# Kernel optimization log

Measured on AMD Instinct MI355X. Metric: run time of the kernel, lower is better.

Reference implementation:

```python
import jax, jax.numpy as jnp
import numpy as np

B_, H_, W_, C_ = 4, 128, 128, 256
HEADS = 8
SPLIT = (8, 32)
POS_DIM = ((C_ // 2) // 4) // 4  # DynamicPosBias(dim//4).pos_dim with dim=C//2 -> 8


def _rel_tables(Hsp, Wsp):
    # rpe_biases: all relative (dy, dx) offsets, shape [(2Hsp-1)*(2Wsp-1), 2]
    gy, gx = np.meshgrid(np.arange(1 - Hsp, Hsp), np.arange(1 - Wsp, Wsp), indexing='ij')
    biases = np.stack([gy.ravel(), gx.ravel()], axis=1).astype(np.float32)
    # relative_position_index: [N, N] lookup into the bias table
    ch, cw = np.meshgrid(np.arange(Hsp), np.arange(Wsp), indexing='ij')
    cf = np.stack([ch.ravel(), cw.ravel()])  # [2, N]
    rel = (cf[:, :, None] - cf[:, None, :]).transpose(1, 2, 0)
    rel[..., 0] += Hsp - 1
    rel[..., 1] += Wsp - 1
    rel[..., 0] *= 2 * Wsp - 1
    idx = rel.sum(-1)
    return jnp.asarray(biases), jnp.asarray(idx)


def _ln(x, g, b):
    m = x.mean(-1, keepdims=True)
    v = ((x - m) ** 2).mean(-1, keepdims=True)
    return (x - m) / jnp.sqrt(v + 1e-5) * g + b


def _dyn_pos(biases, pw, pb, g1, b1, w1, c1, g2, b2, w2, c2, g3, b3, w3, c3):
    # DynamicPosBias, residual=False: pos3(pos2(pos1(pos_proj(b))))
    p = biases @ pw + pb
    p = jax.nn.relu(_ln(p, g1, b1)) @ w1 + c1
    p = jax.nn.relu(_ln(p, g2, b2)) @ w2 + c2
    p = jax.nn.relu(_ln(p, g3, b3)) @ w3 + c3
    return p  # [num_rel, heads]


def _win_attn(q, k, v, Hsp, Wsp, H, W, heads, pos_table, rel_idx):
    B, L, Cb = q.shape
    N = Hsp * Wsp
    hd = Cb // heads
    scale = hd ** (-0.5)

    def part(t):  # (B, L, Cb) -> (B*nW, heads, N, hd)
        t = t.reshape(B, H // Hsp, Hsp, W // Wsp, Wsp, Cb)
        t = t.transpose(0, 1, 3, 2, 4, 5).reshape(-1, N, heads, hd)
        return t.transpose(0, 2, 1, 3)

    qw, kw, vw = part(q) * scale, part(k), part(v)
    attn = jnp.einsum('whnd,whmd->whnm', qw, kw)
    rpb = pos_table[rel_idx.reshape(-1)].reshape(N, N, heads).transpose(2, 0, 1)
    attn = jax.nn.softmax(attn + rpb[None], axis=-1)
    ow = jnp.einsum('whnm,whmd->whnd', attn, vw)
    ow = ow.transpose(0, 2, 1, 3).reshape(-1, N, Cb)
    # windows2img
    img = ow.reshape(B, H // Hsp, W // Wsp, Hsp, Wsp, Cb)
    img = img.transpose(0, 1, 3, 2, 4, 5).reshape(B, H * W, Cb)
    return img


def setup_inputs() -> dict:
    key = jax.random.key(0)
    ks = jax.random.split(key, 16)
    nrm = lambda k, shp: jax.random.normal(k, shp, jnp.float32) * 0.02
    P, hb = POS_DIM, HEADS // 2
    d = {}
    d['x'] = jax.random.normal(ks[0], (B_, H_ * W_, C_), jnp.float32)
    d['w_qkv'] = nrm(ks[1], (C_, 3 * C_))
    d['w_proj'] = nrm(ks[2], (C_, C_))
    d['b_proj'] = jnp.zeros((C_,), jnp.float32)
    d['w_dw'] = nrm(ks[3], (C_, 1, 3, 3))
    d['b_dw'] = jnp.zeros((C_,), jnp.float32)
    d['pp_w'] = nrm(ks[4], (2, 2, P))
    d['pp_b'] = jnp.zeros((2, P), jnp.float32)
    d['ln1_g'] = jnp.ones((2, P), jnp.float32)
    d['ln1_b'] = jnp.zeros((2, P), jnp.float32)
    d['l1_w'] = nrm(ks[5], (2, P, P))
    d['l1_b'] = jnp.zeros((2, P), jnp.float32)
    d['ln2_g'] = jnp.ones((2, P), jnp.float32)
    d['ln2_b'] = jnp.zeros((2, P), jnp.float32)
    d['l2_w'] = nrm(ks[6], (2, P, P))
    d['l2_b'] = jnp.zeros((2, P), jnp.float32)
    d['ln3_g'] = jnp.ones((2, P), jnp.float32)
    d['ln3_b'] = jnp.zeros((2, P), jnp.float32)
    d['l3_w'] = nrm(ks[7], (2, P, hb))
    d['l3_b'] = jnp.zeros((2, hb), jnp.float32)
    d['H'] = H_
    d['W'] = W_
    return d


def reference(x, w_qkv, w_proj, b_proj, w_dw, b_dw, pp_w, pp_b, ln1_g, ln1_b, l1_w, l1_b, ln2_g, ln2_b, l2_w, l2_b, ln3_g, ln3_b, l3_w, l3_b, H, W):
    B, L, C = x.shape
    Cb, hb = C // 2, HEADS // 2
    qkv = (x @ w_qkv).reshape(B, L, 3, C).transpose(2, 0, 1, 3)
    q, k, v = qkv[0], qkv[1], qkv[2]
    v_img = v.transpose(0, 2, 1).reshape(B, C, H, W)
    outs = []
    for br in range(2):  # two cross-shaped window branches (idx=0/1)
        Hsp, Wsp = SPLIT if br == 0 else (SPLIT[1], SPLIT[0])
        sl = slice(br * Cb, (br + 1) * Cb)
        biases, rel_idx = _rel_tables(Hsp, Wsp)
        pos = _dyn_pos(biases, pp_w[br], pp_b[br], ln1_g[br], ln1_b[br], l1_w[br], l1_b[br],
                       ln2_g[br], ln2_b[br], l2_w[br], l2_b[br], ln3_g[br], ln3_b[br], l3_w[br], l3_b[br])
        outs.append(_win_attn(q[..., sl], k[..., sl], v[..., sl], Hsp, Wsp, H, W, hb, pos, rel_idx))
    att = jnp.concatenate(outs, axis=-1)  # (B, L, C)
    # LePE: depthwise 3x3 conv on V (get_v, groups=dim)
    lepe = jax.lax.conv_general_dilated(v_img, w_dw, (1, 1), ((1, 1), (1, 1)),
                                        feature_group_count=C,
                                        dimension_numbers=('NCHW', 'OIHW', 'NCHW'))
    lepe = (lepe + b_dw[None, :, None, None]).transpose(0, 2, 3, 1).reshape(B, L, C)
    return (att + lepe) @ w_proj + b_proj
```

## Files before the change

kernel.cpp:

```cpp
#include <hip/hip_runtime.h>
#include <hip/hip_bf16.h>
#include <math.h>

#define B_ 4
#define HH 128
#define WW 128
#define CC 256
#define LL (HH * WW)
#define NROWS (B_ * LL)
#define NREL 945
#define SCALE 0.17677669529663687f
#define LOG2E 1.4426950408889634f
#define SCALE2 (0.17677669529663687f * 1.4426950408889634f)

typedef __attribute__((ext_vector_type(8))) _Float16 half8;
typedef __attribute__((ext_vector_type(2))) __fp16 fp16x2;
typedef __attribute__((ext_vector_type(4))) float f32x4;

__device__ __forceinline__ unsigned short f2h(float f) {
    union { _Float16 h; unsigned short u; } v;
    v.h = (_Float16)f;
    return v.u;
}
__device__ __forceinline__ float h2f(unsigned short u) {
    union { unsigned short u; _Float16 h; } v;
    v.u = u;
    return (float)v.h;
}
__device__ __forceinline__ float exp2_raw(float x) {
    float r;
    asm("v_exp_f32 %0, %1" : "=v"(r) : "v"(x));
    return r;
}
__device__ __forceinline__ void gl_lds16(const unsigned short* g, unsigned short* l) {
    __builtin_amdgcn_global_load_lds((const __attribute__((address_space(1))) void*)g,
                                     (__attribute__((address_space(3))) void*)l, 16, 0, 0);
}

__device__ inline void ln_relu8(float* v, const float* g, const float* b) {
    float m = 0.f;
#pragma unroll
    for (int j = 0; j < 8; j++) m += v[j];
    m *= 0.125f;
    float var = 0.f;
#pragma unroll
    for (int j = 0; j < 8; j++) { float d = v[j] - m; var += d * d; }
    var *= 0.125f;
    float inv = 1.0f / sqrtf(var + 1e-5f);
#pragma unroll
    for (int j = 0; j < 8; j++) {
        float xn = (v[j] - m) * inv * g[j] + b[j];
        v[j] = xn > 0.f ? xn : 0.f;
    }
}

__device__ inline void mat8x8(const float* in, float* out, const float* w, const float* bias) {
#pragma unroll
    for (int j = 0; j < 8; j++) {
        float s = bias[j];
#pragma unroll
        for (int i = 0; i < 8; i++) s = fmaf(in[i], w[i * 8 + j], s);
        out[j] = s;
    }
}

__global__ void pos_kernel(const float* __restrict__ pp_w, const float* __restrict__ pp_b,
                           const float* __restrict__ ln1_g, const float* __restrict__ ln1_b,
                           const float* __restrict__ l1_w, const float* __restrict__ l1_b,
                           const float* __restrict__ ln2_g, const float* __restrict__ ln2_b,
                           const float* __restrict__ l2_w, const float* __restrict__ l2_b,
                           const float* __restrict__ ln3_g, const float* __restrict__ ln3_b,
                           const float* __restrict__ l3_w, const float* __restrict__ l3_b,
                           float* __restrict__ pos) {
    const int br = blockIdx.x;
    const int Wsp = br ? 8 : 32;
    const int Hsp = br ? 32 : 8;
    const int W2 = 2 * Wsp - 1;
    const int nrel = (2 * Hsp - 1) * W2;
    for (int r = threadIdx.x; r < nrel; r += blockDim.x) {
        float dy = (float)(r / W2 - (Hsp - 1));
        float dx = (float)(r % W2 - (Wsp - 1));
        float p[8], t[8];
#pragma unroll
        for (int j = 0; j < 8; j++)
            p[j] = dy * pp_w[br * 16 + j] + dx * pp_w[br * 16 + 8 + j] + pp_b[br * 8 + j];
        ln_relu8(p, ln1_g + br * 8, ln1_b + br * 8);
        mat8x8(p, t, l1_w + br * 64, l1_b + br * 8);
        ln_relu8(t, ln2_g + br * 8, ln2_b + br * 8);
        mat8x8(t, p, l2_w + br * 64, l2_b + br * 8);
        ln_relu8(p, ln3_g + br * 8, ln3_b + br * 8);
#pragma unroll
        for (int j = 0; j < 4; j++) {
            float s = l3_b[br * 4 + j];
#pragma unroll
            for (int i = 0; i < 8; i++) s = fmaf(p[i], l3_w[br * 32 + i * 4 + j], s);
            pos[(br * NREL + r) * 4 + j] = s;
        }
    }
}

__global__ void rpb_kernel(const float* __restrict__ pos, float* __restrict__ T2) {
    const int m = threadIdx.x;
    const int n = blockIdx.x;
    const int h = blockIdx.y;
    const int br = blockIdx.z;
    const int logW = br ? 3 : 5;
    const int Wsp = 1 << logW;
    const int Hsp = 256 >> logW;
    const int W2 = 2 * Wsp - 1;
    const int i_n = n >> logW, j_n = n & (Wsp - 1);
    const int i_m = m >> logW, j_m = m & (Wsp - 1);
    const int idx = (i_n - i_m + Hsp - 1) * W2 + (j_n - j_m + Wsp - 1);
    float v = pos[(br * NREL + idx) * 4 + h] * LOG2E;
    const int qs = n >> 4;
    const int ks = m >> 4;
    const int lane = ((n >> 2) & 3) * 16 + (m & 15);
    const int i = n & 3;
    T2[((((size_t)(br * 4 + h) * 16 + qs) * 16 + ks) * 64 + lane) * 4 + i] = v;
}

__global__ void convw_kernel(const float* __restrict__ w, unsigned short* __restrict__ th,
                             int Kd, int Nd) {
    int idx = blockIdx.x * blockDim.x + threadIdx.x;
    if (idx >= Kd * Nd) return;
    int n = idx / Kd, k = idx - n * Kd;
    th[idx] = f2h(w[(size_t)k * Nd + n]);
}

__global__ __launch_bounds__(256) void convx_kernel(const float* __restrict__ x,
                                                    unsigned short* __restrict__ xh) {
    size_t i = ((size_t)blockIdx.x * 256 + threadIdx.x) * 4;
    float4 v = *(const float4*)(x + i);
    ushort4 h;
    h.x = f2h(v.x); h.y = f2h(v.y); h.z = f2h(v.z); h.w = f2h(v.w);
    *(ushort4*)(xh + i) = h;
}

__global__ __launch_bounds__(256) void gemm_f16(const unsigned short* __restrict__ A,
                                                const unsigned short* __restrict__ B,
                                                unsigned short* __restrict__ C,
                                                int ldc, int nblk) {
    const int K = 256;
    __shared__ unsigned short sA[4096];
    __shared__ unsigned short sB[4096];

    const int tid = threadIdx.x;
    const int cpx = gridDim.x >> 3;
    const int bid = blockIdx.x;
    const int swz = (bid & 7) * cpx + (bid >> 3);
    const int nb = swz % nblk;
    const int mb = swz / nblk;
    const size_t blockM = (size_t)mb * 128;
    const int blockN = nb * 128;

    const int srow = tid >> 2;
    const int schunk = (tid & 3) * 8;
    const unsigned short* pA = A + (blockM + srow) * K + schunk;
    const unsigned short* pB = B + (size_t)(blockN + srow) * K + schunk;
    const size_t rstep = (size_t)64 * K;

    const int w = tid >> 6;
    const int lane = tid & 63;
    const int quad = lane >> 4;
    const int l15 = lane & 15;
    const int wm = (w & 1) * 64;
    const int wn = (w >> 1) * 64;

    f32x4 acc[4][4];
#pragma unroll
    for (int i = 0; i < 4; i++)
#pragma unroll
        for (int j = 0; j < 4; j++) acc[i][j] = (f32x4){0.f, 0.f, 0.f, 0.f};

    for (int kb = 0; kb < K; kb += 32) {
        gl_lds16(pA + kb, sA + tid * 8);
        gl_lds16(pA + kb + rstep, sA + 2048 + tid * 8);
        gl_lds16(pB + kb, sB + tid * 8);
        gl_lds16(pB + kb + rstep, sB + 2048 + tid * 8);
        __syncthreads();

        half8 fa[4], fb[4];
#pragma unroll
        for (int i = 0; i < 4; i++) {
            fa[i] = *(const half8*)(sA + (wm + i * 16 + l15) * 32 + quad * 8);
            fb[i] = *(const half8*)(sB + (wn + i * 16 + l15) * 32 + quad * 8);
        }
#pragma unroll
        for (int i = 0; i < 4; i++)
#pragma unroll
            for (int j = 0; j < 4; j++)
                acc[i][j] = __builtin_amdgcn_mfma_f32_16x16x32_f16(fa[i], fb[j], acc[i][j], 0, 0, 0);
        __syncthreads();
    }

#pragma unroll
    for (int j = 0; j < 4; j++) {
        int col = blockN + wn + j * 16 + l15;
        float sc = (ldc == 768 && col < 256) ? SCALE2 : 1.0f;
#pragma unroll
        for (int i = 0; i < 4; i++)
#pragma unroll
            for (int r = 0; r < 4; r++) {
                size_t row = blockM + wm + i * 16 + quad * 4 + r;
                C[row * ldc + col] = f2h(acc[i][j][r] * sc);
            }
    }
}

__global__ __launch_bounds__(256) void gemm_proj(const unsigned short* __restrict__ A,
                                                 const unsigned short* __restrict__ B,
                                                 float* __restrict__ C,
                                                 const float* __restrict__ bias) {
    const int K = 256;
    __shared__ unsigned short sA[4096];
    __shared__ unsigned short sB[4096];

    const int tid = threadIdx.x;
    const int cpx = gridDim.x >> 3;
    const int bid = blockIdx.x;
    const int swz = (bid & 7) * cpx + (bid >> 3);
    const int nb = swz & 1;
    const int mb = swz >> 1;
    const size_t blockM = (size_t)mb * 128;
    const int blockN = nb * 128;

    const int srow = tid >> 2;
    const int schunk = (tid & 3) * 8;
    const unsigned short* pA = A + (blockM + srow) * K + schunk;
    const unsigned short* pB = B + (size_t)(blockN + srow) * K + schunk;
    const size_t rstep = (size_t)64 * K;

    const int w = tid >> 6;
    const int lane = tid & 63;
    const int quad = lane >> 4;
    const int l15 = lane & 15;
    const int wm = (w & 1) * 64;
    const int wn = (w >> 1) * 64;

    f32x4 acc[4][4];
#pragma unroll
    for (int i = 0; i < 4; i++)
#pragma unroll
        for (int j = 0; j < 4; j++) acc[i][j] = (f32x4){0.f, 0.f, 0.f, 0.f};

    for (int kb = 0; kb < K; kb += 32) {
        gl_lds16(pA + kb, sA + tid * 8);
        gl_lds16(pA + kb + rstep, sA + 2048 + tid * 8);
        gl_lds16(pB + kb, sB + tid * 8);
        gl_lds16(pB + kb + rstep, sB + 2048 + tid * 8);
        __syncthreads();

        half8 fa[4], fb[4];
#pragma unroll
        for (int i = 0; i < 4; i++) {
            fa[i] = *(const half8*)(sA + (wm + i * 16 + l15) * 32 + quad * 8);
            fb[i] = *(const half8*)(sB + (wn + i * 16 + l15) * 32 + quad * 8);
        }
#pragma unroll
        for (int i = 0; i < 4; i++)
#pragma unroll
            for (int j = 0; j < 4; j++)
                acc[i][j] = __builtin_amdgcn_mfma_f32_16x16x32_f16(fa[i], fb[j], acc[i][j], 0, 0, 0);
        __syncthreads();
    }

#pragma unroll
    for (int j = 0; j < 4; j++) {
        int col = blockN + wn + j * 16 + l15;
        float bv = bias[col];
#pragma unroll
        for (int i = 0; i < 4; i++)
#pragma unroll
            for (int r = 0; r < 4; r++) {
                size_t row = blockM + wm + i * 16 + quad * 4 + r;
                C[row * 256 + col] = acc[i][j][r] + bv;
            }
    }
}

__global__ __launch_bounds__(256) void attn_mfma(const unsigned short* __restrict__ qkvb,
                                                 const float* __restrict__ T2,
                                                 unsigned short* __restrict__ attb) {
    __shared__ unsigned short Ks[256][32];
    __shared__ unsigned short Vt[32][264];
    __shared__ unsigned int   Pc[4][16][20];

    const int tid = threadIdx.x;
    const int wi = blockIdx.x;
    const int h = blockIdx.y;
    const int br = blockIdx.z;
    const int logW = br ? 3 : 5;
    const int Wsp = 1 << logW;
    const int Hsp = 256 >> logW;
    const int logNWx = br ? 4 : 2;
    const int b = wi >> 6;
    const int win = wi & 63;
    const int wy = win >> logNWx;
    const int wx = win & ((1 << logNWx) - 1);
    const int ccol = br * 128 + h * 32;

#pragma unroll
    for (int it = 0; it < 8; ++it) {
        int n = it * 32 + (tid >> 3);
        int d4 = (tid & 7) * 4;
        int iy = n >> logW, ix = n & (Wsp - 1);
        size_t row = ((size_t)b * LL + (wy * Hsp + iy) * WW + wx * Wsp + ix) * 768;
        ushort4 kv = *(const ushort4*)(qkvb + row + 256 + ccol + d4);
        ushort4 vv = *(const ushort4*)(qkvb + row + 512 + ccol + d4);
        *(ushort4*)&Ks[n][d4] = kv;
        int pos = (n & ~31) + 2 * (n & 15) + ((n >> 4) & 1);
        Vt[d4 + 0][pos] = vv.x;
        Vt[d4 + 1][pos] = vv.y;
        Vt[d4 + 2][pos] = vv.z;
        Vt[d4 + 3][pos] = vv.w;
    }
    __syncthreads();

    const int w = tid >> 6;
    const int lane = tid & 63;
    const int quad = lane >> 4;
    const int l15 = lane & 15;
    const f32x4 zero = {0.f, 0.f, 0.f, 0.f};

#pragma unroll 1
    for (int qt = 0; qt < 4; ++qt) {
        const int qbase = qt * 64 + w * 16;
        const int qrow = qbase + l15;
        const int iyq = qrow >> logW, ixq = qrow & (Wsp - 1);
        const size_t qpix = (size_t)b * LL + (wy * Hsp + iyq) * WW + wx * Wsp + ixq;
        half8 qfrag = *(const half8*)(qkvb + qpix * 768 + ccol + quad * 8);

        const float* Tf = T2 + (((size_t)(br * 4 + h) * 16 + (qt * 4 + w)) * 16) * 256 + lane * 4;

        f32x4 o0 = zero, o1 = zero;
        float rsum[4] = {0.f, 0.f, 0.f, 0.f};

#pragma unroll 2
        for (int kc = 0; kc < 8; ++kc) {
            const int kb0 = kc * 32;
            f32x4 b0 = *(const f32x4*)(Tf + (size_t)(kc * 2) * 256);
            f32x4 b1 = *(const f32x4*)(Tf + (size_t)(kc * 2 + 1) * 256);
            half8 kf0 = *(const half8*)&Ks[kb0 + l15][quad * 8];
            half8 kf1 = *(const half8*)&Ks[kb0 + 16 + l15][quad * 8];
            f32x4 s0 = __builtin_amdgcn_mfma_f32_16x16x32_f16(qfrag, kf0, b0, 0, 0, 0);
            f32x4 s1 = __builtin_amdgcn_mfma_f32_16x16x32_f16(qfrag, kf1, b1, 0, 0, 0);
#pragma unroll
            for (int i = 0; i < 4; ++i) {
                float e0 = exp2_raw(s0[i]);
                float e1 = exp2_raw(s1[i]);
                rsum[i] += e0 + e1;
                union { fp16x2 h; unsigned u; } cv;
                cv.h = __builtin_amdgcn_cvt_pkrtz(e0, e1);
                Pc[w][quad * 4 + i][l15] = cv.u;
            }
            half8 pf = *(const half8*)&Pc[w][l15][quad * 4];
            half8 vf0 = *(const half8*)&Vt[l15][kb0 + quad * 8];
            half8 vf1 = *(const half8*)&Vt[16 + l15][kb0 + quad * 8];
            o0 = __builtin_amdgcn_mfma_f32_16x16x32_f16(pf, vf0, o0, 0, 0, 0);
            o1 = __builtin_amdgcn_mfma_f32_16x16x32_f16(pf, vf1, o1, 0, 0, 0);
        }

#pragma unroll
        for (int i = 0; i < 4; ++i) {
            float s = rsum[i];
            s += __shfl_xor(s, 1, 64);
            s += __shfl_xor(s, 2, 64);
            s += __shfl_xor(s, 4, 64);
            s += __shfl_xor(s, 8, 64);
            rsum[i] = 1.0f / s;
        }

#pragma unroll
        for (int i = 0; i < 4; ++i) {
            int r = qbase + quad * 4 + i;
            int iyr = r >> logW, ixr = r & (Wsp - 1);
            size_t pix = (size_t)b * LL + (wy * Hsp + iyr) * WW + wx * Wsp + ixr;
            unsigned short* op = attb + pix * 256 + ccol;
            op[l15] = f2h(o0[i] * rsum[i]);
            op[16 + l15] = f2h(o1[i] * rsum[i]);
        }
    }
}

__global__ __launch_bounds__(256) void lepe_kernel(const unsigned short* __restrict__ qkvb,
                                                   const float* __restrict__ w_dw,
                                                   const float* __restrict__ b_dw,
                                                   unsigned short* __restrict__ attb) {
    const int lane = threadIdx.x & 63;
    const int wv = threadIdx.x >> 6;
    const int c4 = lane * 4;
    const int gid = blockIdx.x * 4 + wv;
    const int ys = gid & 7;
    const int x  = (gid >> 3) & 127;
    const int b  = gid >> 10;
    const int y0 = ys * 16;

    float wreg[36];
    const float* wp = w_dw + c4 * 9;
#pragma unroll
    for (int q = 0; q < 9; q++) {
        float4 t = *(const float4*)(wp + q * 4);
        wreg[q * 4 + 0] = t.x; wreg[q * 4 + 1] = t.y;
        wreg[q * 4 + 2] = t.z; wreg[q * 4 + 3] = t.w;
    }
    const float4 bv = *(const float4*)(b_dw + c4);
    const float4 z4 = {0.f, 0.f, 0.f, 0.f};
    const bool xm_ok = (x > 0), xp_ok = (x < 127);

    const unsigned short* vp = qkvb + (((size_t)b << 14) + x) * 768 + 512 + c4;

    float4 r0[3], r1[3], r2[3];

#define LDV(yy, dx, dst) { \
        ushort4 u = *(const ushort4*)(vp + (ptrdiff_t)(yy) * 98304 + (dx) * 768); \
        dst.x = h2f(u.x); dst.y = h2f(u.y); dst.z = h2f(u.z); dst.w = h2f(u.w); }
#define LDROW(yy, d) { \
        if ((yy) < 0 || (yy) > 127) { d[0] = z4; d[1] = z4; d[2] = z4; } \
        else { \
            if (xm_ok) LDV(yy, -1, d[0]) else d[0] = z4; \
            LDV(yy, 0, d[1]); \
            if (xp_ok) LDV(yy, 1, d[2]) else d[2] = z4; } }
#define TAP(rv, j) \
        acc.x = fmaf(rv.x, wreg[0 * 9 + (j)], acc.x); \
        acc.y = fmaf(rv.y, wreg[1 * 9 + (j)], acc.y); \
        acc.z = fmaf(rv.z, wreg[2 * 9 + (j)], acc.z); \
        acc.w = fmaf(rv.w, wreg[3 * 9 + (j)], acc.w);

    LDROW(y0 - 1, r0)
    LDROW(y0, r1)

#pragma unroll
    for (int t = 0; t < 16; ++t) {
        const int y = y0 + t;
        LDROW(y + 1, r2)

        const size_t opx = ((((size_t)b << 14) + y * 128 + x) << 8) + c4;
        ushort4 av = *(const ushort4*)(attb + opx);
        float4 acc;
        acc.x = h2f(av.x) + bv.x; acc.y = h2f(av.y) + bv.y;
        acc.z = h2f(av.z) + bv.z; acc.w = h2f(av.w) + bv.w;

        TAP(r0[0], 0) TAP(r0[1], 1) TAP(r0[2], 2)
        TAP(r1[0], 3) TAP(r1[1], 4) TAP(r1[2], 5)
        TAP(r2[0], 6) TAP(r2[1], 7) TAP(r2[2], 8)

        ushort4 o;
        o.x = f2h(acc.x); o.y = f2h(acc.y); o.z = f2h(acc.z); o.w = f2h(acc.w);
        *(ushort4*)(attb + opx) = o;

        r0[0] = r1[0]; r0[1] = r1[1]; r0[2] = r1[2];
        r1[0] = r2[0]; r1[1] = r2[1]; r1[2] = r2[2];
    }
#undef LDV
#undef LDROW
#undef TAP
}

extern "C" void kernel_launch(void* const* d_in, const int* in_sizes, int n_in,
                              void* d_out, int out_size, void* d_ws, size_t ws_size,
                              hipStream_t stream) {
    const float* x     = (const float*)d_in[0];
    const float* w_qkv = (const float*)d_in[1];
    const float* w_proj= (const float*)d_in[2];
    const float* b_proj= (const float*)d_in[3];
    const float* w_dw  = (const float*)d_in[4];
    const float* b_dw  = (const float*)d_in[5];
    const float* pp_w  = (const float*)d_in[6];
    const float* pp_b  = (const float*)d_in[7];
    const float* ln1_g = (const float*)d_in[8];
    const float* ln1_b = (const float*)d_in[9];
    const float* l1_w  = (const float*)d_in[10];
    const float* l1_b  = (const float*)d_in[11];
    const float* ln2_g = (const float*)d_in[12];
    const float* ln2_b = (const float*)d_in[13];
    const float* l2_w  = (const float*)d_in[14];
    const float* l2_b  = (const float*)d_in[15];
    const float* ln3_g = (const float*)d_in[16];
    const float* ln3_b = (const float*)d_in[17];
    const float* l3_w  = (const float*)d_in[18];
    const float* l3_b  = (const float*)d_in[19];

    float* pos = (float*)d_ws;
    float* T2  = pos + 7680;
    unsigned short* qkvb = (unsigned short*)(T2 + 524288);
    unsigned short* attb = qkvb + (size_t)NROWS * 768;
    unsigned short* xh   = attb + (size_t)NROWS * 256;
    unsigned short* wqh  = xh + (size_t)NROWS * 256;
    unsigned short* wph  = wqh + 768 * 256;

    pos_kernel<<<2, 128, 0, stream>>>(pp_w, pp_b, ln1_g, ln1_b, l1_w, l1_b,
                                      ln2_g, ln2_b, l2_w, l2_b, ln3_g, ln3_b,
                                      l3_w, l3_b, pos);
    rpb_kernel<<<dim3(256, 4, 2), 256, 0, stream>>>(pos, T2);
    convw_kernel<<<768, 256, 0, stream>>>(w_qkv, wqh, 256, 768);
    convw_kernel<<<256, 256, 0, stream>>>(w_proj, wph, 256, 256);
    convx_kernel<<<NROWS / 4, 256, 0, stream>>>(x, xh);
    gemm_f16<<<(NROWS / 128) * 6, 256, 0, stream>>>(xh, wqh, qkvb, 768, 6);
    attn_mfma<<<dim3(256, 4, 2), 256, 0, stream>>>(qkvb, T2, attb);
    lepe_kernel<<<1024, 256, 0, stream>>>(qkvb, w_dw, b_dw, attb);
    gemm_proj<<<(NROWS / 128) * 2, 256, 0, stream>>>(attb, wph, (float*)d_out, b_proj);
}
```

Measured before the change: 327.2 us.

## Compute transposed attention scores so P stays in registers, skipping LDS round trip

Swaps the MFMA operand order so S^T = K·Q^T is computed, which puts each query's scores in a layout that can be packed straight into the B operand of the PV MFMA. This removes the per-iteration shared-memory write and read of the probability tile (Pc) and the LDS traffic that came with it. The bias table and the V column permutation are re-laid out to match the new fragment ordering. Row sums now need only two cross-lane shuffles, and the output is written as vectorized ushort4 stores. The risk is that the remapped bias table or V permutation does not match the fragment layout exactly.

```diff
diff --git a/kernel.cpp b/kernel.cpp
--- a/kernel.cpp
+++ b/kernel.cpp
@@ -112,11 +112,15 @@
     const int i_m = m >> logW, j_m = m & (Wsp - 1);
     const int idx = (i_n - i_m + Hsp - 1) * W2 + (j_n - j_m + Wsp - 1);
     float v = pos[(br * NREL + idx) * 4 + h] * LOG2E;
-    const int qs = n >> 4;
-    const int ks = m >> 4;
-    const int lane = ((n >> 2) & 3) * 16 + (m & 15);
-    const int i = n & 3;
-    T2[((((size_t)(br * 4 + h) * 16 + qs) * 16 + ks) * 64 + lane) * 4 + i] = v;
+    const int qchunk = n >> 4;
+    const int l15q = n & 15;
+    const int kc = m >> 5;
+    const int lk = m & 31;
+    const int s = (lk >> 4) & 1;
+    const int quad = (lk & 15) >> 2;
+    const int i = lk & 3;
+    const int lane = quad * 16 + l15q;
+    T2[(((size_t)(br * 4 + h) * 16 + qchunk) * 4096) + ((kc * 2 + s) * 256) + lane * 4 + i] = v;
 }
 
 __global__ void convw_kernel(const float* __restrict__ w, unsigned short* __restrict__ th,
@@ -283,7 +287,6 @@
                                                  unsigned short* __restrict__ attb) {
     __shared__ unsigned short Ks[256][32];
     __shared__ unsigned short Vt[32][264];
-    __shared__ unsigned int   Pc[4][16][20];
 
     const int tid = threadIdx.x;
     const int wi = blockIdx.x;
@@ -308,7 +311,7 @@
         ushort4 kv = *(const ushort4*)(qkvb + row + 256 + ccol + d4);
         ushort4 vv = *(const ushort4*)(qkvb + row + 512 + ccol + d4);
         *(ushort4*)&Ks[n][d4] = kv;
-        int pos = (n & ~31) + 2 * (n & 15) + ((n >> 4) & 1);
+        int pos = (n & ~31) + (((n & 12) << 1) | ((n & 16) >> 2) | (n & 3));
         Vt[d4 + 0][pos] = vv.x;
         Vt[d4 + 1][pos] = vv.y;
         Vt[d4 + 2][pos] = vv.z;
@@ -330,55 +333,49 @@
         const size_t qpix = (size_t)b * LL + (wy * Hsp + iyq) * WW + wx * Wsp + ixq;
         half8 qfrag = *(const half8*)(qkvb + qpix * 768 + ccol + quad * 8);
 
-        const float* Tf = T2 + (((size_t)(br * 4 + h) * 16 + (qt * 4 + w)) * 16) * 256 + lane * 4;
+        const float* Tf = T2 + ((size_t)(br * 4 + h) * 16 + (qt * 4 + w)) * 4096 + lane * 4;
 
         f32x4 o0 = zero, o1 = zero;
-        float rsum[4] = {0.f, 0.f, 0.f, 0.f};
+        float rsum = 0.f;
 
 #pragma unroll 2
         for (int kc = 0; kc < 8; ++kc) {
             const int kb0 = kc * 32;
-            f32x4 b0 = *(const f32x4*)(Tf + (size_t)(kc * 2) * 256);
-            f32x4 b1 = *(const f32x4*)(Tf + (size_t)(kc * 2 + 1) * 256);
+            f32x4 b0 = *(const f32x4*)(Tf + kc * 512);
+            f32x4 b1 = *(const f32x4*)(Tf + kc * 512 + 256);
             half8 kf0 = *(const half8*)&Ks[kb0 + l15][quad * 8];
             half8 kf1 = *(const half8*)&Ks[kb0 + 16 + l15][quad * 8];
-            f32x4 s0 = __builtin_amdgcn_mfma_f32_16x16x32_f16(qfrag, kf0, b0, 0, 0, 0);
-            f32x4 s1 = __builtin_amdgcn_mfma_f32_16x16x32_f16(qfrag, kf1, b1, 0, 0, 0);
-#pragma unroll
-            for (int i = 0; i < 4; ++i) {
-                float e0 = exp2_raw(s0[i]);
-                float e1 = exp2_raw(s1[i]);
-                rsum[i] += e0 + e1;
-                union { fp16x2 h; unsigned u; } cv;
-                cv.h = __builtin_amdgcn_cvt_pkrtz(e0, e1);
-                Pc[w][quad * 4 + i][l15] = cv.u;
-            }
-            half8 pf = *(const half8*)&Pc[w][l15][quad * 4];
+            f32x4 s0 = __builtin_amdgcn_mfma_f32_16x16x32_f16(kf0, qfrag, b0, 0, 0, 0);
+            f32x4 s1 = __builtin_amdgcn_mfma_f32_16x16x32_f16(kf1, qfrag, b1, 0, 0, 0);
+            float e00 = exp2_raw(s0[0]), e01 = exp2_raw(s0[1]);
+            float e02 = exp2_raw(s0[2]), e03 = exp2_raw(s0[3]);
+            float e10 = exp2_raw(s1[0]), e11 = exp2_raw(s1[1]);
+            float e12 = exp2_raw(s1[2]), e13 = exp2_raw(s1[3]);
+            rsum += ((e00 + e01) + (e02 + e03)) + ((e10 + e11) + (e12 + e13));
+            union { half8 h; unsigned u[4]; } pt;
+            union { fp16x2 h; unsigned u; } cv;
+            cv.h = __builtin_amdgcn_cvt_pkrtz(e00, e01); pt.u[0] = cv.u;
+            cv.h = __builtin_amdgcn_cvt_pkrtz(e02, e03); pt.u[1] = cv.u;
+            cv.h = __builtin_amdgcn_cvt_pkrtz(e10, e11); pt.u[2] = cv.u;
+            cv.h = __builtin_amdgcn_cvt_pkrtz(e12, e13); pt.u[3] = cv.u;
             half8 vf0 = *(const half8*)&Vt[l15][kb0 + quad * 8];
             half8 vf1 = *(const half8*)&Vt[16 + l15][kb0 + quad * 8];
-            o0 = __builtin_amdgcn_mfma_f32_16x16x32_f16(pf, vf0, o0, 0, 0, 0);
-            o1 = __builtin_amdgcn_mfma_f32_16x16x32_f16(pf, vf1, o1, 0, 0, 0);
+            o0 = __builtin_amdgcn_mfma_f32_16x16x32_f16(vf0, pt.h, o0, 0, 0, 0);
+            o1 = __builtin_amdgcn_mfma_f32_16x16x32_f16(vf1, pt.h, o1, 0, 0, 0);
         }
 
-#pragma unroll
-        for (int i = 0; i < 4; ++i) {
-            float s = rsum[i];
-            s += __shfl_xor(s, 1, 64);
-            s += __shfl_xor(s, 2, 64);
-            s += __shfl_xor(s, 4, 64);
-            s += __shfl_xor(s, 8, 64);
-            rsum[i] = 1.0f / s;
-        }
-
-#pragma unroll
-        for (int i = 0; i < 4; ++i) {
-            int r = qbase + quad * 4 + i;
-            int iyr = r >> logW, ixr = r & (Wsp - 1);
-            size_t pix = (size_t)b * LL + (wy * Hsp + iyr) * WW + wx * Wsp + ixr;
-            unsigned short* op = attb + pix * 256 + ccol;
-            op[l15] = f2h(o0[i] * rsum[i]);
-            op[16 + l15] = f2h(o1[i] * rsum[i]);
-        }
+        rsum += __shfl_xor(rsum, 16, 64);
+        rsum += __shfl_xor(rsum, 32, 64);
+        const float rinv = 1.0f / rsum;
+
+        unsigned short* op = attb + qpix * 256 + ccol;
+        ushort4 w0, w1;
+        w0.x = f2h(o0[0] * rinv); w0.y = f2h(o0[1] * rinv);
+        w0.z = f2h(o0[2] * rinv); w0.w = f2h(o0[3] * rinv);
+        w1.x = f2h(o1[0] * rinv); w1.y = f2h(o1[1] * rinv);
+        w1.z = f2h(o1[2] * rinv); w1.w = f2h(o1[3] * rinv);
+        *(ushort4*)(op + quad * 4) = w0;
+        *(ushort4*)(op + 16 + quad * 4) = w1;
     }
 }
 
```

Measured after the change: 315.6 us. -3.5%, faster.
